# Performance work log

Measured on AMD Instinct MI355X. Metric: run time of the kernel, lower is better.

The kernel has to match this reference:

```python
import jax, jax.numpy as jnp
import numpy as np

EPS = 1e-12

def _spectral_normalize(W, u):
    # torch spectral_norm (eval-time math): v = normalize(W^T u), sigma = u^T W v
    u = jax.lax.stop_gradient(u)
    v = W.T @ u
    v = jax.lax.stop_gradient(v / (jnp.linalg.norm(v) + EPS))
    sigma = u @ (W @ v)
    return W / sigma

def _conv1x1(x, W):
    # 1x1 conv, no bias: (out,in) x (B,in,H,W) -> (B,out,H,W)
    return jnp.einsum('oc,bchw->bohw', W, x)

def setup_inputs() -> dict:
    key = jax.random.key(0)
    ks = jax.random.split(key, 10)
    B, C, H, W = 4, 512, 64, 64
    Cp = C // 8
    return {
        'x': jax.random.normal(ks[0], (B, C, H, W), jnp.float32),
        'Wf': jax.random.normal(ks[1], (Cp, C), jnp.float32) * 0.05,
        'Wg': jax.random.normal(ks[2], (Cp, C), jnp.float32) * 0.05,
        'Wh': jax.random.normal(ks[3], (Cp, C), jnp.float32) * 0.05,
        'Wv': jax.random.normal(ks[4], (C, Cp), jnp.float32) * 0.05,
        'uf': jax.random.normal(ks[5], (Cp,), jnp.float32),
        'ug': jax.random.normal(ks[6], (Cp,), jnp.float32),
        'uh': jax.random.normal(ks[7], (Cp,), jnp.float32),
        'uv': jax.random.normal(ks[8], (C,), jnp.float32),
        'gamma': jax.random.normal(ks[9], (1,), jnp.float32) * 0.1,
    }

def reference(x, Wf, Wg, Wh, Wv, uf, ug, uh, uv, gamma):
    B, C, H, W = x.shape
    Cp = Wf.shape[0]
    N = H * W
    Wf_sn = _spectral_normalize(Wf, uf)
    Wg_sn = _spectral_normalize(Wg, ug)
    Wh_sn = _spectral_normalize(Wh, uh)
    Wv_sn = _spectral_normalize(Wv, uv)
    fx = _conv1x1(x, Wf_sn).reshape(B, Cp, N)   # (B,Cp,N)
    gx = _conv1x1(x, Wg_sn).reshape(B, Cp, N)   # (B,Cp,N)
    # fx^T gx: (B,N,N), unscaled single-head attention, softmax over last dim
    scores = jnp.einsum('bcn,bcm->bnm', fx, gx)
    attn = jax.nn.softmax(scores, axis=-1)
    hx = _conv1x1(x, Wh_sn).reshape(B, Cp, N)
    # hx @ attn: out[b,c,j] = sum_i hx[b,c,i] * attn[b,i,j]
    out = jnp.einsum('bci,bij->bcj', hx, attn).reshape(B, Cp, H, W)
    unscaled = _conv1x1(out, Wv_sn)
    return gamma * unscaled + x
```

## Files before the change

### kernel.cpp

```cpp
#include <hip/hip_runtime.h>


#define NB 4
#define CC 512
#define CP 64
#define NN 4096

typedef __attribute__((ext_vector_type(8))) short short8;
typedef __attribute__((ext_vector_type(4))) float floatx4;
typedef __attribute__((ext_vector_type(16))) float floatx16;

#define MFMA32(A, B, C) __builtin_amdgcn_mfma_f32_32x32x16_bf16((A), (B), (C), 0, 0, 0)

__device__ __forceinline__ float bf2f_u(unsigned short h) {
    return __uint_as_float((unsigned)h << 16);
}
__device__ __forceinline__ float bf16lo(unsigned v) { return __uint_as_float(v << 16); }
__device__ __forceinline__ float bf16hi(unsigned v) { return __uint_as_float(v & 0xffff0000u); }
__device__ __forceinline__ unsigned short f2bf(float f) {
    unsigned u = __float_as_uint(f);
    u += 0x7fffu + ((u >> 16) & 1u);
    return (unsigned short)(u >> 16);
}
__device__ __forceinline__ unsigned pack2bf(float a, float b) {
    return (unsigned)f2bf(a) | ((unsigned)f2bf(b) << 16);
}
__device__ __forceinline__ float ldS(const void* p, long i, int f32) {
    return f32 ? ((const float*)p)[i] : bf2f_u(((const unsigned short*)p)[i]);
}
__device__ __forceinline__ float2 ld2(const void* p, long i, int f32) {
    if (f32) return *reinterpret_cast<const float2*>((const float*)p + i);
    unsigned v = *reinterpret_cast<const unsigned*>((const unsigned short*)p + i);
    return make_float2(bf16lo(v), bf16hi(v));
}
__device__ __forceinline__ float4 ld4(const void* p, long i, int f32) {
    if (f32) return *reinterpret_cast<const float4*>((const float*)p + i);
    uint2 v = *reinterpret_cast<const uint2*>((const unsigned short*)p + i);
    return make_float4(bf16lo(v.x), bf16hi(v.x), bf16lo(v.y), bf16hi(v.y));
}
__device__ __forceinline__ short8 frag8(const void* p, long i, int f32) {
    uint4 au;
    if (f32) {
        float4 v0 = *reinterpret_cast<const float4*>((const float*)p + i);
        float4 v1 = *reinterpret_cast<const float4*>((const float*)p + i + 4);
        au.x = pack2bf(v0.x, v0.y); au.y = pack2bf(v0.z, v0.w);
        au.z = pack2bf(v1.x, v1.y); au.w = pack2bf(v1.z, v1.w);
    } else {
        au = *reinterpret_cast<const uint4*>((const unsigned short*)p + i);
    }
    return *reinterpret_cast<short8*>(&au);
}
__device__ __forceinline__ short8 as_s8(uint4 v) { return *reinterpret_cast<short8*>(&v); }
__device__ __forceinline__ floatx16 zero16() {
    floatx16 z;
    #pragma unroll
    for (int i = 0; i < 16; ++i) z[i] = 0.f;
    return z;
}
__device__ __forceinline__ unsigned cvtpk_bf16(float a, float b) {
    unsigned r;
    asm("v_cvt_pk_bf16_f32 %0, %1, %2" : "=v"(r) : "v"(a), "v"(b));
    return r;
}
__device__ __forceinline__ void pl32swap(unsigned &a, unsigned &b) {
    asm("v_permlane32_swap_b32 %0, %1" : "+v"(a), "+v"(b));
}
__device__ __forceinline__ float rcpf(float x) {
    float r;
    asm("v_rcp_f32 %0, %1" : "=v"(r) : "v"(x));
    return r;
}

__global__ __launch_bounds__(256) void detect_kernel(
    const unsigned* __restrict__ x, int* __restrict__ flag)
{
    __shared__ int red[256];
    const int t = threadIdx.x;
    int bad = 0;
    for (int i = t; i < 4096; i += 256) {
        unsigned w = x[i];
        float f0 = __uint_as_float(w << 16);
        float f1 = __uint_as_float(w & 0xffff0000u);
        float a0 = fabsf(f0), a1 = fabsf(f1);
        if (!(a0 <= 1e3f) || (f0 != 0.f && a0 < 1e-20f)) bad++;
        if (!(a1 <= 1e3f) || (f1 != 0.f && a1 < 1e-20f)) bad++;
    }
    red[t] = bad;
    __syncthreads();
    for (int s = 128; s > 0; s >>= 1) { if (t < s) red[t] += red[t + s]; __syncthreads(); }
    if (t == 0) *flag = (red[0] > 64) ? 1 : 0;
}

__global__ __launch_bounds__(512) void sigma_kernel(
    const void* __restrict__ Wf, const void* __restrict__ Wg,
    const void* __restrict__ Wh, const void* __restrict__ Wv,
    const void* __restrict__ uf, const void* __restrict__ ug,
    const void* __restrict__ uh, const void* __restrict__ uv,
    const int* __restrict__ dflag, float* __restrict__ sig)
{
    const int f32 = *dflag;
    const int w = blockIdx.x;
    const void* W;
    const void* u;
    if (w == 0)      { W = Wf; u = uf; }
    else if (w == 1) { W = Wg; u = ug; }
    else if (w == 2) { W = Wh; u = uh; }
    else             { W = Wv; u = uv; }

    __shared__ float us[512];
    __shared__ float red[512];
    const int t = threadIdx.x;
    float S;

    if (w < 3) {
        if (t < 64) us[t] = ldS(u, t, f32);
        __syncthreads();
        float a = 0.f;
        #pragma unroll
        for (int i = 0; i < 64; ++i)
            a = fmaf(ldS(W, (long)i * 512 + t, f32), us[i], a);
        red[t] = a * a;
        __syncthreads();
        #pragma unroll
        for (int s = 256; s > 0; s >>= 1) {
            if (t < s) red[t] += red[t + s];
            __syncthreads();
        }
        S = red[0];
    } else {
        us[t] = ldS(u, t, f32);
        __syncthreads();
        const int g = t >> 6, c = t & 63;
        float a = 0.f;
        #pragma unroll
        for (int k = 0; k < 64; ++k) {
            int i = g + k * 8;
            a = fmaf(ldS(W, (long)i * 64 + c, f32), us[i], a);
        }
        red[t] = a;
        __syncthreads();
        #pragma unroll
        for (int s = 256; s >= 64; s >>= 1) {
            if (t < s) red[t] += red[t + s];
            __syncthreads();
        }
        float ac = (t < 64) ? red[t] : 0.f;
        __syncthreads();
        red[t] = ac * ac;
        __syncthreads();
        #pragma unroll
        for (int s = 256; s > 0; s >>= 1) {
            if (t < s) red[t] += red[t + s];
            __syncthreads();
        }
        S = red[0];
    }
    if (t == 0) sig[w] = (sqrtf(S) + 1e-12f) / S;
}

__global__ __launch_bounds__(256) void proj_kernel(
    const void* __restrict__ x,
    const void* __restrict__ Wf,
    const void* __restrict__ Wg,
    const void* __restrict__ Wh,
    const int* __restrict__ dflag,
    const float* __restrict__ sig,
    unsigned short* __restrict__ fxF, unsigned short* __restrict__ gxF,
    unsigned short* __restrict__ hxF)
{
    const int f32 = *dflag;
    const int n0 = blockIdx.x * 64;
    const int b  = blockIdx.y;
    const int wi = blockIdx.z;
    const void* __restrict__ W = (wi == 0) ? Wf : ((wi == 1) ? Wg : Wh);
    const float scale = sig[wi];

    __shared__ unsigned short Wl[64][72];

    const int t = threadIdx.x;
    const int wv = t >> 6, l = t & 63, l15 = l & 15, quad = l >> 4;
    const int n = n0 + 16 * wv + l15;

    floatx4 acc[4];
    #pragma unroll
    for (int ct = 0; ct < 4; ++ct) acc[ct] = (floatx4){0.f, 0.f, 0.f, 0.f};

    for (int kc = 0; kc < CC; kc += 64) {
        #pragma unroll
        for (int idx = t; idx < 2048; idx += 256) {
            int c  = idx >> 5;
            int kk = (idx & 31) * 2;
            float2 v = ld2(W, (long)c * CC + kc + kk, f32);
            *reinterpret_cast<unsigned*>(&Wl[c][kk]) = pack2bf(v.x * scale, v.y * scale);
        }
        __syncthreads();

        #pragma unroll
        for (int ks = 0; ks < 2; ++ks) {
            const int kbase = kc + ks * 32 + quad * 8;
            float xv[8];
            #pragma unroll
            for (int j = 0; j < 8; ++j)
                xv[j] = ldS(x, ((long)b * CC + kbase + j) * NN + n, f32);
            uint4 au;
            au.x = pack2bf(xv[0], xv[1]); au.y = pack2bf(xv[2], xv[3]);
            au.z = pack2bf(xv[4], xv[5]); au.w = pack2bf(xv[6], xv[7]);
            short8 a = *reinterpret_cast<short8*>(&au);
            #pragma unroll
            for (int ct = 0; ct < 4; ++ct) {
                short8 bfr = *reinterpret_cast<const short8*>(
                    &Wl[ct * 16 + l15][ks * 32 + quad * 8]);
                acc[ct] = __builtin_amdgcn_mfma_f32_16x16x32_bf16(a, bfr, acc[ct], 0, 0, 0);
            }
        }
        __syncthreads();
    }

    if (wi < 2) {
        unsigned short* __restrict__ dstF = (wi == 0) ? fxF : gxF;
        const int nloc = 16 * wv + quad * 4;
        #pragma unroll
        for (int ct = 0; ct < 4; ++ct)
            #pragma unroll
            for (int r = 0; r < 4; ++r) {
                int nn = n0 + nloc + r;
                size_t off = (((size_t)(b * 128 + (nn >> 5)) * 4 + ct) * 64
                              + (l15 >> 3) * 32 + (nn & 31)) * 8 + (l15 & 7);
                dstF[off] = f2bf(acc[ct][r]);
            }
    } else {
        const int tile = (n0 + 16 * wv) >> 5;
        const int ich  = wv & 1;
        const int ksub = quad >> 1;
        const int ebase = (quad & 1) * 4;
        #pragma unroll
        for (int ct = 0; ct < 4; ++ct) {
            int part = ct >> 1;
            int lloc = ksub * 32 + (ct & 1) * 16 + l15;
            size_t off = ((((size_t)(b * 128 + tile) * 2 + ich) * 2 + part) * 64
                          + lloc) * 8 + ebase;
            uint2 o;
            o.x = pack2bf(acc[ct][0], acc[ct][1]);
            o.y = pack2bf(acc[ct][2], acc[ct][3]);
            *reinterpret_cast<uint2*>(&hxF[off]) = o;
        }
    }
}

__global__ __launch_bounds__(256, 4) void rowstats_kernel(
    const unsigned short* __restrict__ fxF, const unsigned short* __restrict__ gxF,
    float* __restrict__ rl)
{
    const int t = threadIdx.x;
    const int w = t >> 6, l = t & 63, l31 = l & 31, hi = l >> 5;
    const int b = blockIdx.z;
    const int i0 = blockIdx.x * 128 + w * 32;
    const int jbase = blockIdx.y * (NN / 8);

    const unsigned short* fA = fxF + ((size_t)(b * 128 + (i0 >> 5))) * 2048 + (size_t)l * 8;
    uint4 af[4];
    #pragma unroll
    for (int kc = 0; kc < 4; ++kc)
        af[kc] = *reinterpret_cast<const uint4*>(fA + kc * 512);

    const unsigned short* gB = gxF + ((size_t)(b * 128 + (jbase >> 5))) * 2048 + (size_t)l * 8;

    float suml[16];
    #pragma unroll
    for (int r = 0; r < 16; ++r) suml[r] = 0.f;

    uint4 bf0[4], bf1[4];
    auto loadB = [&](uint4* bf, int jt) {
        const unsigned short* p = gB + (size_t)jt * 2048;
        #pragma unroll
        for (int kc = 0; kc < 4; ++kc)
            bf[kc] = *reinterpret_cast<const uint4*>(p + kc * 512);
    };
    auto bodyR = [&](uint4* bf) {
        floatx16 s = zero16();
        #pragma unroll
        for (int kc = 0; kc < 4; ++kc)
            s = MFMA32(as_s8(af[kc]), as_s8(bf[kc]), s);
        #pragma unroll
        for (int r = 0; r < 16; ++r) suml[r] += __expf(s[r]);
    };

    loadB(bf0, 0);
    for (int jt = 0; jt < 16; jt += 2) {
        loadB(bf1, jt + 1);
        bodyR(bf0);
        if (jt + 2 < 16) loadB(bf0, jt + 2);
        bodyR(bf1);
    }

    #pragma unroll
    for (int r = 0; r < 16; ++r) {
        float v = suml[r];
        v += __shfl_xor(v, 1);
        v += __shfl_xor(v, 2);
        v += __shfl_xor(v, 4);
        v += __shfl_xor(v, 8);
        v += __shfl_xor(v, 16);
        suml[r] = v;
    }
    if (l31 == 0) {
        #pragma unroll
        for (int r = 0; r < 16; ++r) {
            int row = (r & 3) + 8 * (r >> 2) + 4 * hi;
            atomicAdd(&rl[(size_t)b * NN + i0 + row], suml[r]);
        }
    }
}

__global__ __launch_bounds__(256, 2) void pv_kernel(
    const unsigned short* __restrict__ fxF, const unsigned short* __restrict__ gxF,
    const unsigned short* __restrict__ hxF, const float* __restrict__ rl,
    float* __restrict__ opT0, float* __restrict__ opT1)
{
    const int t = threadIdx.x;
    const int w = t >> 6, l = t & 63, l31 = l & 31, hi = l >> 5;
    const int b = blockIdx.z;
    const int j0 = blockIdx.x * 64;
    const int isb = blockIdx.y;
    const int ibase = isb * (NN / 2) + w * (NN / 8);

    __shared__ float red[64 * 64];

    uint4 qf0[4], qf1[4];
    {
        const unsigned short* gq = gxF + ((size_t)(b * 128 + (j0 >> 5))) * 2048 + (size_t)l * 8;
        #pragma unroll
        for (int kc = 0; kc < 4; ++kc) {
            qf0[kc] = *reinterpret_cast<const uint4*>(gq + kc * 512);
            qf1[kc] = *reinterpret_cast<const uint4*>(gq + 2048 + kc * 512);
        }
    }

    floatx16 acc00 = zero16(), acc01 = zero16();
    floatx16 acc10 = zero16(), acc11 = zero16();

    const unsigned short* fb = fxF + ((size_t)(b * 128 + (ibase >> 5))) * 2048 + (size_t)l * 8;
    const unsigned short* vb = hxF + ((size_t)(b * 128 + (ibase >> 5))) * 2048 + (size_t)l * 8;
    const float* rbase = rl + (size_t)b * NN + ibase + (hi << 2);

    uint4 af0[4], af1[4], vf[4];
    auto loadA = [&](uint4* af, int it) {
        const unsigned short* p = fb + (size_t)it * 2048;
        #pragma unroll
        for (int kc = 0; kc < 4; ++kc)
            af[kc] = *reinterpret_cast<const uint4*>(p + kc * 512);
    };
    auto loadV = [&](int it) {
        const unsigned short* p = vb + (size_t)it * 2048;
        vf[0] = *reinterpret_cast<const uint4*>(p);
        vf[1] = *reinterpret_cast<const uint4*>(p + 1024);
        vf[2] = *reinterpret_cast<const uint4*>(p + 512);
        vf[3] = *reinterpret_cast<const uint4*>(p + 1536);
    };
    auto body = [&](uint4* af, int it) {
        const float* rp = rbase + it * 32;
        float4 rv0 = *reinterpret_cast<const float4*>(rp);
        float4 rv1 = *reinterpret_cast<const float4*>(rp + 8);
        float4 rv2 = *reinterpret_cast<const float4*>(rp + 16);
        float4 rv3 = *reinterpret_cast<const float4*>(rp + 24);
        float ri[16];
        ri[0] = rcpf(rv0.x); ri[1] = rcpf(rv0.y); ri[2] = rcpf(rv0.z); ri[3] = rcpf(rv0.w);
        ri[4] = rcpf(rv1.x); ri[5] = rcpf(rv1.y); ri[6] = rcpf(rv1.z); ri[7] = rcpf(rv1.w);
        ri[8] = rcpf(rv2.x); ri[9] = rcpf(rv2.y); ri[10] = rcpf(rv2.z); ri[11] = rcpf(rv2.w);
        ri[12] = rcpf(rv3.x); ri[13] = rcpf(rv3.y); ri[14] = rcpf(rv3.z); ri[15] = rcpf(rv3.w);
        #pragma unroll
        for (int sub = 0; sub < 2; ++sub) {
            uint4* qf = sub ? qf1 : qf0;
            floatx16 s = zero16();
            #pragma unroll
            for (int kc = 0; kc < 4; ++kc)
                s = MFMA32(as_s8(af[kc]), as_s8(qf[kc]), s);
            float e[16];
            #pragma unroll
            for (int r = 0; r < 16; ++r) e[r] = __expf(s[r]) * ri[r];
            unsigned u0 = cvtpk_bf16(e[0], e[1]);
            unsigned u1 = cvtpk_bf16(e[2], e[3]);
            unsigned u2 = cvtpk_bf16(e[4], e[5]);
            unsigned u3 = cvtpk_bf16(e[6], e[7]);
            pl32swap(u0, u2);
            pl32swap(u1, u3);
            uint4 pa0 = make_uint4(u0, u1, u2, u3);
            unsigned u4 = cvtpk_bf16(e[8], e[9]);
            unsigned u5 = cvtpk_bf16(e[10], e[11]);
            unsigned u6 = cvtpk_bf16(e[12], e[13]);
            unsigned u7 = cvtpk_bf16(e[14], e[15]);
            pl32swap(u4, u6);
            pl32swap(u5, u7);
            uint4 pa1 = make_uint4(u4, u5, u6, u7);
            floatx16& a0 = sub ? acc10 : acc00;
            floatx16& a1 = sub ? acc11 : acc01;
            a0 = MFMA32(as_s8(pa0), as_s8(vf[0]), a0);
            a0 = MFMA32(as_s8(pa1), as_s8(vf[1]), a0);
            a1 = MFMA32(as_s8(pa0), as_s8(vf[2]), a1);
            a1 = MFMA32(as_s8(pa1), as_s8(vf[3]), a1);
        }
    };

    loadA(af0, 0);
    for (int it = 0; it < 16; it += 2) {
        loadV(it);
        loadA(af1, it + 1);
        body(af0, it);
        loadV(it + 1);
        if (it + 2 < 16) loadA(af0, it + 2);
        body(af1, it + 1);
    }

    #pragma unroll
    for (int q = 0; q < 4; ++q)
        *reinterpret_cast<float4*>(&red[(q * 256 + t) * 4]) = make_float4(0.f, 0.f, 0.f, 0.f);
    __syncthreads();
    #pragma unroll
    for (int r = 0; r < 16; ++r) {
        int row = (r & 3) + 8 * (r >> 2) + 4 * hi;
        atomicAdd(&red[row * 64 + l31],              acc00[r]);
        atomicAdd(&red[row * 64 + 32 + l31],         acc01[r]);
        atomicAdd(&red[(32 + row) * 64 + l31],       acc10[r]);
        atomicAdd(&red[(32 + row) * 64 + 32 + l31],  acc11[r]);
    }
    __syncthreads();
    float* dst = (isb ? opT1 : opT0) + ((size_t)b * NN + j0) * CP;
    #pragma unroll
    for (int q = 0; q < 4; ++q) {
        int o = (q * 256 + t) * 4;
        *reinterpret_cast<float4*>(dst + o) = *reinterpret_cast<const float4*>(&red[o]);
    }
}

__global__ __launch_bounds__(256) void outproj_kernel(
    const void* __restrict__ x,
    const void* __restrict__ Wv,
    const void* __restrict__ gamma,
    const int* __restrict__ dflag,
    const float* __restrict__ sig,
    const float* __restrict__ opT0,
    const float* __restrict__ opT1,
    void* __restrict__ y)
{
    const int f32 = *dflag;
    const int n0     = blockIdx.x * 64;
    const int cobase = blockIdx.y * 128;
    const int b      = blockIdx.z;
    const int t = threadIdx.x;
    const int wv = t >> 6, l = t & 63, l15 = l & 15, quad = l >> 4;
    const float scale = ldS(gamma, 0, f32) * sig[3];

    floatx4 acc[4][2];
    #pragma unroll
    for (int ns = 0; ns < 4; ++ns)
        #pragma unroll
        for (int ct = 0; ct < 2; ++ct) acc[ns][ct] = (floatx4){0.f, 0.f, 0.f, 0.f};

    #pragma unroll
    for (int ks = 0; ks < 2; ++ks) {
        const int kb = ks * 32 + quad * 8;
        short8 a[4];
        #pragma unroll
        for (int ns = 0; ns < 4; ++ns) {
            const long off = ((long)b * NN + n0 + 16 * ns + l15) * CP + kb;
            float4 x0 = *reinterpret_cast<const float4*>(opT0 + off);
            float4 x1 = *reinterpret_cast<const float4*>(opT0 + off + 4);
            float4 y0 = *reinterpret_cast<const float4*>(opT1 + off);
            float4 y1 = *reinterpret_cast<const float4*>(opT1 + off + 4);
            uint4 au;
            au.x = pack2bf(x0.x + y0.x, x0.y + y0.y);
            au.y = pack2bf(x0.z + y0.z, x0.w + y0.w);
            au.z = pack2bf(x1.x + y1.x, x1.y + y1.y);
            au.w = pack2bf(x1.z + y1.z, x1.w + y1.w);
            a[ns] = *reinterpret_cast<short8*>(&au);
        }
        #pragma unroll
        for (int ct = 0; ct < 2; ++ct) {
            const int co = cobase + 32 * wv + 16 * ct + l15;
            short8 bfr = frag8(Wv, (long)co * CP + kb, f32);
            #pragma unroll
            for (int ns = 0; ns < 4; ++ns)
                acc[ns][ct] = __builtin_amdgcn_mfma_f32_16x16x32_bf16(a[ns], bfr, acc[ns][ct], 0, 0, 0);
        }
    }

    #pragma unroll
    for (int ns = 0; ns < 4; ++ns)
        #pragma unroll
        for (int ct = 0; ct < 2; ++ct) {
            const int co = cobase + 32 * wv + 16 * ct + l15;
            const long base = ((long)b * CC + co) * NN + n0 + 16 * ns + quad * 4;
            float4 xv = ld4(x, base, f32);
            float o0 = fmaf(scale, acc[ns][ct][0], xv.x);
            float o1 = fmaf(scale, acc[ns][ct][1], xv.y);
            float o2 = fmaf(scale, acc[ns][ct][2], xv.z);
            float o3 = fmaf(scale, acc[ns][ct][3], xv.w);
            if (f32) {
                *reinterpret_cast<float4*>((float*)y + base) = make_float4(o0, o1, o2, o3);
            } else {
                uint2 o;
                o.x = pack2bf(o0, o1);
                o.y = pack2bf(o2, o3);
                *reinterpret_cast<uint2*>((unsigned short*)y + base) = o;
            }
        }
}

extern "C" void kernel_launch(void* const* d_in, const int* in_sizes, int n_in,
                              void* d_out, int out_size, void* d_ws, size_t ws_size,
                              hipStream_t stream)
{
    const void* x  = d_in[0];
    const void* Wf = d_in[1];
    const void* Wg = d_in[2];
    const void* Wh = d_in[3];
    const void* Wv = d_in[4];
    const void* uf = d_in[5];
    const void* ug = d_in[6];
    const void* uh = d_in[7];
    const void* uv = d_in[8];
    const void* gm = d_in[9];

    char* base = (char*)d_ws;
    int*   dfl = (int*)(base);
    float* sig = (float*)(base + 512);
    float* rl  = (float*)(base + 1024);
    float* opT0 = (float*)(base + 1024 + 65536);
    float* opT1 = opT0 + (size_t)NB * NN * CP;
    unsigned short* fxF = (unsigned short*)(opT1 + (size_t)NB * NN * CP);
    unsigned short* gxF = fxF + (size_t)NB * CP * NN;
    unsigned short* hxF = gxF + (size_t)NB * CP * NN;

    hipMemsetAsync(rl, 0, (size_t)NB * NN * sizeof(float), stream);

    hipLaunchKernelGGL(detect_kernel, dim3(1), dim3(256), 0, stream,
                       (const unsigned*)x, dfl);
    hipLaunchKernelGGL(sigma_kernel, dim3(4), dim3(512), 0, stream,
                       Wf, Wg, Wh, Wv, uf, ug, uh, uv, dfl, sig);
    hipLaunchKernelGGL(proj_kernel, dim3(NN / 64, NB, 3), dim3(256), 0, stream,
                       x, Wf, Wg, Wh, dfl, sig, fxF, gxF, hxF);
    hipLaunchKernelGGL(rowstats_kernel, dim3(NN / 128, 8, NB), dim3(256), 0, stream,
                       fxF, gxF, rl);
    hipLaunchKernelGGL(pv_kernel, dim3(NN / 64, 2, NB), dim3(256), 0, stream,
                       fxF, gxF, hxF, rl, opT0, opT1);
    hipLaunchKernelGGL(outproj_kernel, dim3(NN / 64, CC / 128, NB), dim3(256), 0, stream,
                       x, Wv, gm, dfl, sig, opT0, opT1, d_out);
}
```

Before: 244.4 us.

## Fuse projections, fold log2e and row normalization into hx, split PV wider

The projection kernel now computes f, g and h in one launch, so x is read once instead of three times. Wf is pre-scaled by log2(e) so the softmax exponent can use the raw v_exp_f32 (exp2) instruction. The per-row 1/rowsum is folded into hx by a new small scale kernel, which removes the reciprocal and multiply from the PV inner loop. PV is split into four i-slices with lighter per-wave state and higher occupancy, at the cost of four partial-output buffers that the output projection must sum, plus an extra launch and extra bf16 rounding of hx.

```diff
diff --git a/kernel.cpp b/kernel.cpp
--- a/kernel.cpp
+++ b/kernel.cpp
@@ -5,6 +5,7 @@
 #define CC 512
 #define CP 64
 #define NN 4096
+#define L2E 1.4426950408889634f
 
 typedef __attribute__((ext_vector_type(8))) short short8;
 typedef __attribute__((ext_vector_type(4))) float floatx4;
@@ -68,6 +69,11 @@
 __device__ __forceinline__ float rcpf(float x) {
     float r;
     asm("v_rcp_f32 %0, %1" : "=v"(r) : "v"(x));
+    return r;
+}
+__device__ __forceinline__ float exp2a(float x) {
+    float r;
+    asm("v_exp_f32 %0, %1" : "=v"(r) : "v"(x));
     return r;
 }
 
@@ -171,27 +177,35 @@
     const int f32 = *dflag;
     const int n0 = blockIdx.x * 64;
     const int b  = blockIdx.y;
-    const int wi = blockIdx.z;
-    const void* __restrict__ W = (wi == 0) ? Wf : ((wi == 1) ? Wg : Wh);
-    const float scale = sig[wi];
-
-    __shared__ unsigned short Wl[64][72];
+
+    __shared__ unsigned short Wl[3][64][72];
 
     const int t = threadIdx.x;
     const int wv = t >> 6, l = t & 63, l15 = l & 15, quad = l >> 4;
     const int n = n0 + 16 * wv + l15;
 
-    floatx4 acc[4];
-    #pragma unroll
-    for (int ct = 0; ct < 4; ++ct) acc[ct] = (floatx4){0.f, 0.f, 0.f, 0.f};
+    float sc[3];
+    sc[0] = sig[0] * L2E;
+    sc[1] = sig[1];
+    sc[2] = sig[2];
+    const void* Ws[3] = {Wf, Wg, Wh};
+
+    floatx4 acc[3][4];
+    #pragma unroll
+    for (int wi = 0; wi < 3; ++wi)
+        #pragma unroll
+        for (int ct = 0; ct < 4; ++ct) acc[wi][ct] = (floatx4){0.f, 0.f, 0.f, 0.f};
 
     for (int kc = 0; kc < CC; kc += 64) {
         #pragma unroll
-        for (int idx = t; idx < 2048; idx += 256) {
-            int c  = idx >> 5;
-            int kk = (idx & 31) * 2;
-            float2 v = ld2(W, (long)c * CC + kc + kk, f32);
-            *reinterpret_cast<unsigned*>(&Wl[c][kk]) = pack2bf(v.x * scale, v.y * scale);
+        for (int idx = t; idx < 6144; idx += 256) {
+            int wi  = idx >> 11;
+            int rem = idx & 2047;
+            int c   = rem >> 5;
+            int kk  = (rem & 31) * 2;
+            float2 v = ld2(Ws[wi], (long)c * CC + kc + kk, f32);
+            *reinterpret_cast<unsigned*>(&Wl[wi][c][kk]) =
+                pack2bf(v.x * sc[wi], v.y * sc[wi]);
         }
         __syncthreads();
 
@@ -207,16 +221,20 @@
             au.z = pack2bf(xv[4], xv[5]); au.w = pack2bf(xv[6], xv[7]);
             short8 a = *reinterpret_cast<short8*>(&au);
             #pragma unroll
-            for (int ct = 0; ct < 4; ++ct) {
-                short8 bfr = *reinterpret_cast<const short8*>(
-                    &Wl[ct * 16 + l15][ks * 32 + quad * 8]);
-                acc[ct] = __builtin_amdgcn_mfma_f32_16x16x32_bf16(a, bfr, acc[ct], 0, 0, 0);
-            }
-        }
-        __syncthreads();
-    }
-
-    if (wi < 2) {
+            for (int wi = 0; wi < 3; ++wi)
+                #pragma unroll
+                for (int ct = 0; ct < 4; ++ct) {
+                    short8 bfr = *reinterpret_cast<const short8*>(
+                        &Wl[wi][ct * 16 + l15][ks * 32 + quad * 8]);
+                    acc[wi][ct] = __builtin_amdgcn_mfma_f32_16x16x32_bf16(
+                        a, bfr, acc[wi][ct], 0, 0, 0);
+                }
+        }
+        __syncthreads();
+    }
+
+    #pragma unroll
+    for (int wi = 0; wi < 2; ++wi) {
         unsigned short* __restrict__ dstF = (wi == 0) ? fxF : gxF;
         const int nloc = 16 * wv + quad * 4;
         #pragma unroll
@@ -226,9 +244,10 @@
                 int nn = n0 + nloc + r;
                 size_t off = (((size_t)(b * 128 + (nn >> 5)) * 4 + ct) * 64
                               + (l15 >> 3) * 32 + (nn & 31)) * 8 + (l15 & 7);
-                dstF[off] = f2bf(acc[ct][r]);
+                dstF[off] = f2bf(acc[wi][ct][r]);
             }
-    } else {
+    }
+    {
         const int tile = (n0 + 16 * wv) >> 5;
         const int ich  = wv & 1;
         const int ksub = quad >> 1;
@@ -240,8 +259,8 @@
             size_t off = ((((size_t)(b * 128 + tile) * 2 + ich) * 2 + part) * 64
                           + lloc) * 8 + ebase;
             uint2 o;
-            o.x = pack2bf(acc[ct][0], acc[ct][1]);
-            o.y = pack2bf(acc[ct][2], acc[ct][3]);
+            o.x = pack2bf(acc[2][ct][0], acc[2][ct][1]);
+            o.y = pack2bf(acc[2][ct][2], acc[2][ct][3]);
             *reinterpret_cast<uint2*>(&hxF[off]) = o;
         }
     }
@@ -282,7 +301,7 @@
         for (int kc = 0; kc < 4; ++kc)
             s = MFMA32(as_s8(af[kc]), as_s8(bf[kc]), s);
         #pragma unroll
-        for (int r = 0; r < 16; ++r) suml[r] += __expf(s[r]);
+        for (int r = 0; r < 16; ++r) suml[r] += exp2a(s[r]);
     };
 
     loadB(bf0, 0);
@@ -312,123 +331,127 @@
     }
 }
 
-__global__ __launch_bounds__(256, 2) void pv_kernel(
+__global__ __launch_bounds__(256) void scalehx_kernel(
+    const float* __restrict__ rl, unsigned short* __restrict__ hxF)
+{
+    const int idx = blockIdx.x * 256 + threadIdx.x;
+    const int l = idx & 63;
+    const int r = idx >> 6;
+    const int ich = (r >> 1) & 1;
+    const int tile = (r >> 2) & 127;
+    const int b = r >> 9;
+    const int i0 = tile * 32 + ich * 16 + (l >> 5) * 8;
+    const float* rp = rl + (size_t)b * NN + i0;
+    float4 ra = *reinterpret_cast<const float4*>(rp);
+    float4 rb = *reinterpret_cast<const float4*>(rp + 4);
+    uint4 v = *reinterpret_cast<uint4*>(hxF + (size_t)idx * 8);
+    uint4 ov;
+    ov.x = pack2bf(bf16lo(v.x) * rcpf(ra.x), bf16hi(v.x) * rcpf(ra.y));
+    ov.y = pack2bf(bf16lo(v.y) * rcpf(ra.z), bf16hi(v.y) * rcpf(ra.w));
+    ov.z = pack2bf(bf16lo(v.z) * rcpf(rb.x), bf16hi(v.z) * rcpf(rb.y));
+    ov.w = pack2bf(bf16lo(v.w) * rcpf(rb.z), bf16hi(v.w) * rcpf(rb.w));
+    *reinterpret_cast<uint4*>(hxF + (size_t)idx * 8) = ov;
+}
+
+__global__ __launch_bounds__(256, 4) void pv_kernel(
     const unsigned short* __restrict__ fxF, const unsigned short* __restrict__ gxF,
-    const unsigned short* __restrict__ hxF, const float* __restrict__ rl,
-    float* __restrict__ opT0, float* __restrict__ opT1)
+    const unsigned short* __restrict__ hxF,
+    float* __restrict__ opF0, float* __restrict__ opF1,
+    float* __restrict__ opF2, float* __restrict__ opF3)
 {
     const int t = threadIdx.x;
     const int w = t >> 6, l = t & 63, l31 = l & 31, hi = l >> 5;
+    const int igrp = w >> 1, jgrp = w & 1;
     const int b = blockIdx.z;
     const int j0 = blockIdx.x * 64;
     const int isb = blockIdx.y;
-    const int ibase = isb * (NN / 2) + w * (NN / 8);
+    const int tbase = isb * 32 + igrp * 16;
 
     __shared__ float red[64 * 64];
 
-    uint4 qf0[4], qf1[4];
+    uint4 qf[4];
     {
-        const unsigned short* gq = gxF + ((size_t)(b * 128 + (j0 >> 5))) * 2048 + (size_t)l * 8;
-        #pragma unroll
-        for (int kc = 0; kc < 4; ++kc) {
-            qf0[kc] = *reinterpret_cast<const uint4*>(gq + kc * 512);
-            qf1[kc] = *reinterpret_cast<const uint4*>(gq + 2048 + kc * 512);
-        }
-    }
-
-    floatx16 acc00 = zero16(), acc01 = zero16();
-    floatx16 acc10 = zero16(), acc11 = zero16();
-
-    const unsigned short* fb = fxF + ((size_t)(b * 128 + (ibase >> 5))) * 2048 + (size_t)l * 8;
-    const unsigned short* vb = hxF + ((size_t)(b * 128 + (ibase >> 5))) * 2048 + (size_t)l * 8;
-    const float* rbase = rl + (size_t)b * NN + ibase + (hi << 2);
-
-    uint4 af0[4], af1[4], vf[4];
-    auto loadA = [&](uint4* af, int it) {
-        const unsigned short* p = fb + (size_t)it * 2048;
+        const unsigned short* gq =
+            gxF + ((size_t)(b * 128 + (j0 >> 5) + jgrp)) * 2048 + (size_t)l * 8;
         #pragma unroll
         for (int kc = 0; kc < 4; ++kc)
-            af[kc] = *reinterpret_cast<const uint4*>(p + kc * 512);
-    };
-    auto loadV = [&](int it) {
-        const unsigned short* p = vb + (size_t)it * 2048;
-        vf[0] = *reinterpret_cast<const uint4*>(p);
-        vf[1] = *reinterpret_cast<const uint4*>(p + 1024);
-        vf[2] = *reinterpret_cast<const uint4*>(p + 512);
-        vf[3] = *reinterpret_cast<const uint4*>(p + 1536);
-    };
-    auto body = [&](uint4* af, int it) {
-        const float* rp = rbase + it * 32;
-        float4 rv0 = *reinterpret_cast<const float4*>(rp);
-        float4 rv1 = *reinterpret_cast<const float4*>(rp + 8);
-        float4 rv2 = *reinterpret_cast<const float4*>(rp + 16);
-        float4 rv3 = *reinterpret_cast<const float4*>(rp + 24);
-        float ri[16];
-        ri[0] = rcpf(rv0.x); ri[1] = rcpf(rv0.y); ri[2] = rcpf(rv0.z); ri[3] = rcpf(rv0.w);
-        ri[4] = rcpf(rv1.x); ri[5] = rcpf(rv1.y); ri[6] = rcpf(rv1.z); ri[7] = rcpf(rv1.w);
-        ri[8] = rcpf(rv2.x); ri[9] = rcpf(rv2.y); ri[10] = rcpf(rv2.z); ri[11] = rcpf(rv2.w);
-        ri[12] = rcpf(rv3.x); ri[13] = rcpf(rv3.y); ri[14] = rcpf(rv3.z); ri[15] = rcpf(rv3.w);
-        #pragma unroll
-        for (int sub = 0; sub < 2; ++sub) {
-            uint4* qf = sub ? qf1 : qf0;
-            floatx16 s = zero16();
-            #pragma unroll
-            for (int kc = 0; kc < 4; ++kc)
-                s = MFMA32(as_s8(af[kc]), as_s8(qf[kc]), s);
-            float e[16];
-            #pragma unroll
-            for (int r = 0; r < 16; ++r) e[r] = __expf(s[r]) * ri[r];
-            unsigned u0 = cvtpk_bf16(e[0], e[1]);
-            unsigned u1 = cvtpk_bf16(e[2], e[3]);
-            unsigned u2 = cvtpk_bf16(e[4], e[5]);
-            unsigned u3 = cvtpk_bf16(e[6], e[7]);
-            pl32swap(u0, u2);
-            pl32swap(u1, u3);
-            uint4 pa0 = make_uint4(u0, u1, u2, u3);
-            unsigned u4 = cvtpk_bf16(e[8], e[9]);
-            unsigned u5 = cvtpk_bf16(e[10], e[11]);
-            unsigned u6 = cvtpk_bf16(e[12], e[13]);
-            unsigned u7 = cvtpk_bf16(e[14], e[15]);
-            pl32swap(u4, u6);
-            pl32swap(u5, u7);
-            uint4 pa1 = make_uint4(u4, u5, u6, u7);
-            floatx16& a0 = sub ? acc10 : acc00;
-            floatx16& a1 = sub ? acc11 : acc01;
-            a0 = MFMA32(as_s8(pa0), as_s8(vf[0]), a0);
-            a0 = MFMA32(as_s8(pa1), as_s8(vf[1]), a0);
-            a1 = MFMA32(as_s8(pa0), as_s8(vf[2]), a1);
-            a1 = MFMA32(as_s8(pa1), as_s8(vf[3]), a1);
-        }
-    };
-
-    loadA(af0, 0);
-    for (int it = 0; it < 16; it += 2) {
-        loadV(it);
-        loadA(af1, it + 1);
-        body(af0, it);
-        loadV(it + 1);
-        if (it + 2 < 16) loadA(af0, it + 2);
-        body(af1, it + 1);
+            qf[kc] = *reinterpret_cast<const uint4*>(gq + kc * 512);
+    }
+
+    floatx16 acc0 = zero16(), acc1 = zero16();
+
+    const unsigned short* fb = fxF + ((size_t)(b * 128 + tbase)) * 2048 + (size_t)l * 8;
+    const unsigned short* vb = hxF + ((size_t)(b * 128 + tbase)) * 2048 + (size_t)l * 8;
+
+    #pragma unroll 2
+    for (int it = 0; it < 16; ++it) {
+        const unsigned short* fp = fb + (size_t)it * 2048;
+        const unsigned short* vp = vb + (size_t)it * 2048;
+        uint4 af[4], vf[4];
+        #pragma unroll
+        for (int kc = 0; kc < 4; ++kc)
+            af[kc] = *reinterpret_cast<const uint4*>(fp + kc * 512);
+        vf[0] = *reinterpret_cast<const uint4*>(vp);
+        vf[1] = *reinterpret_cast<const uint4*>(vp + 1024);
+        vf[2] = *reinterpret_cast<const uint4*>(vp + 512);
+        vf[3] = *reinterpret_cast<const uint4*>(vp + 1536);
+
+        floatx16 s = zero16();
+        #pragma unroll
+        for (int kc = 0; kc < 4; ++kc)
+            s = MFMA32(as_s8(af[kc]), as_s8(qf[kc]), s);
+
+        float e[16];
+        #pragma unroll
+        for (int r = 0; r < 16; ++r) e[r] = exp2a(s[r]);
+
+        unsigned u0 = cvtpk_bf16(e[0], e[1]);
+        unsigned u1 = cvtpk_bf16(e[2], e[3]);
+        unsigned u2 = cvtpk_bf16(e[4], e[5]);
+        unsigned u3 = cvtpk_bf16(e[6], e[7]);
+        pl32swap(u0, u2);
+        pl32swap(u1, u3);
+        uint4 pa0 = make_uint4(u0, u1, u2, u3);
+        unsigned u4 = cvtpk_bf16(e[8], e[9]);
+        unsigned u5 = cvtpk_bf16(e[10], e[11]);
+        unsigned u6 = cvtpk_bf16(e[12], e[13]);
+        unsigned u7 = cvtpk_bf16(e[14], e[15]);
+        pl32swap(u4, u6);
+        pl32swap(u5, u7);
+        uint4 pa1 = make_uint4(u4, u5, u6, u7);
+
+        acc0 = MFMA32(as_s8(pa0), as_s8(vf[0]), acc0);
+        acc0 = MFMA32(as_s8(pa1), as_s8(vf[1]), acc0);
+        acc1 = MFMA32(as_s8(pa0), as_s8(vf[2]), acc1);
+        acc1 = MFMA32(as_s8(pa1), as_s8(vf[3]), acc1);
     }
 
     #pragma unroll
     for (int q = 0; q < 4; ++q)
-        *reinterpret_cast<float4*>(&red[(q * 256 + t) * 4]) = make_float4(0.f, 0.f, 0.f, 0.f);
+        *reinterpret_cast<float4*>(&red[(q * 256 + t) * 4]) =
+            make_float4(0.f, 0.f, 0.f, 0.f);
     __syncthreads();
     #pragma unroll
     for (int r = 0; r < 16; ++r) {
-        int row = (r & 3) + 8 * (r >> 2) + 4 * hi;
-        atomicAdd(&red[row * 64 + l31],              acc00[r]);
-        atomicAdd(&red[row * 64 + 32 + l31],         acc01[r]);
-        atomicAdd(&red[(32 + row) * 64 + l31],       acc10[r]);
-        atomicAdd(&red[(32 + row) * 64 + 32 + l31],  acc11[r]);
+        int row = jgrp * 32 + (r & 3) + 8 * (r >> 2) + 4 * hi;
+        atomicAdd(&red[row * 64 + l31],      acc0[r]);
+        atomicAdd(&red[row * 64 + 32 + l31], acc1[r]);
     }
     __syncthreads();
-    float* dst = (isb ? opT1 : opT0) + ((size_t)b * NN + j0) * CP;
+
+    float* __restrict__ dst = (isb == 0) ? opF0 : ((isb == 1) ? opF1 : ((isb == 2) ? opF2 : opF3));
     #pragma unroll
     for (int q = 0; q < 4; ++q) {
-        int o = (q * 256 + t) * 4;
-        *reinterpret_cast<float4*>(dst + o) = *reinterpret_cast<const float4*>(&red[o]);
+        int idx = q * 256 + t;
+        int e2  = idx & 1;
+        int ll  = (idx >> 1) & 63;
+        int ks  = (idx >> 7) & 1;
+        int ntl = idx >> 8;
+        int jloc = ntl * 16 + (ll & 15);
+        int cp   = ks * 32 + ((ll >> 4) << 3) + e2 * 4;
+        float4 v = *reinterpret_cast<const float4*>(&red[jloc * 64 + cp]);
+        size_t off = (((size_t)(b * 256 + (j0 >> 4) + ntl) * 2 + ks) * 64 + ll) * 8 + e2 * 4;
+        *reinterpret_cast<float4*>(dst + off) = v;
     }
 }
 
@@ -438,8 +461,8 @@
     const void* __restrict__ gamma,
     const int* __restrict__ dflag,
     const float* __restrict__ sig,
-    const float* __restrict__ opT0,
-    const float* __restrict__ opT1,
+    const float* __restrict__ opF0, const float* __restrict__ opF1,
+    const float* __restrict__ opF2, const float* __restrict__ opF3,
     void* __restrict__ y)
 {
     const int f32 = *dflag;
@@ -458,29 +481,40 @@
 
     #pragma unroll
     for (int ks = 0; ks < 2; ++ks) {
+        short8 a[4];
+        #pragma unroll
+        for (int ns = 0; ns < 4; ++ns) {
+            size_t fo = (((size_t)(b * 256 + (n0 >> 4) + ns) * 2 + ks) * 64 + l) * 8;
+            float4 s0 = *reinterpret_cast<const float4*>(opF0 + fo);
+            float4 s1 = *reinterpret_cast<const float4*>(opF1 + fo);
+            float4 s2 = *reinterpret_cast<const float4*>(opF2 + fo);
+            float4 s3 = *reinterpret_cast<const float4*>(opF3 + fo);
+            float4 t0 = *reinterpret_cast<const float4*>(opF0 + fo + 4);
+            float4 t1 = *reinterpret_cast<const float4*>(opF1 + fo + 4);
+            float4 t2 = *reinterpret_cast<const float4*>(opF2 + fo + 4);
+            float4 t3 = *reinterpret_cast<const float4*>(opF3 + fo + 4);
+            float v0 = s0.x + s1.x + s2.x + s3.x;
+            float v1 = s0.y + s1.y + s2.y + s3.y;
+            float v2 = s0.z + s1.z + s2.z + s3.z;
+            float v3 = s0.w + s1.w + s2.w + s3.w;
+            float v4 = t0.x + t1.x + t2.x + t3.x;
+            float v5 = t0.y + t1.y + t2.y + t3.y;
+            float v6 = t0.z + t1.z + t2.z + t3.z;
+            float v7 = t0.w + t1.w + t2.w + t3.w;
+            uint4 au;
+            au.x = pack2bf(v0, v1); au.y = pack2bf(v2, v3);
+            au.z = pack2bf(v4, v5); au.w = pack2bf(v6, v7);
+            a[ns] = *reinterpret_cast<short8*>(&au);
+        }
         const int kb = ks * 32 + quad * 8;
-        short8 a[4];
-        #pragma unroll
-        for (int ns = 0; ns < 4; ++ns) {
-            const long off = ((long)b * NN + n0 + 16 * ns + l15) * CP + kb;
-            float4 x0 = *reinterpret_cast<const float4*>(opT0 + off);
-            float4 x1 = *reinterpret_cast<const float4*>(opT0 + off + 4);
-            float4 y0 = *reinterpret_cast<const float4*>(opT1 + off);
-            float4 y1 = *reinterpret_cast<const float4*>(opT1 + off + 4);
-            uint4 au;
-            au.x = pack2bf(x0.x + y0.x, x0.y + y0.y);
-            au.y = pack2bf(x0.z + y0.z, x0.w + y0.w);
-            au.z = pack2bf(x1.x + y1.x, x1.y + y1.y);
-            au.w = pack2bf(x1.z + y1.z, x1.w + y1.w);
-            a[ns] = *reinterpret_cast<short8*>(&au);
-        }
         #pragma unroll
         for (int ct = 0; ct < 2; ++ct) {
             const int co = cobase + 32 * wv + 16 * ct + l15;
             short8 bfr = frag8(Wv, (long)co * CP + kb, f32);
             #pragma unroll
             for (int ns = 0; ns < 4; ++ns)
-                acc[ns][ct] = __builtin_amdgcn_mfma_f32_16x16x32_bf16(a[ns], bfr, acc[ns][ct], 0, 0, 0);
+                acc[ns][ct] = __builtin_amdgcn_mfma_f32_16x16x32_bf16(
+                    a[ns], bfr, acc[ns][ct], 0, 0, 0);
         }
     }
 
@@ -525,9 +559,11 @@
     int*   dfl = (int*)(base);
     float* sig = (float*)(base + 512);
     float* rl  = (float*)(base + 1024);
-    float* opT0 = (float*)(base + 1024 + 65536);
-    float* opT1 = opT0 + (size_t)NB * NN * CP;
-    unsigned short* fxF = (unsigned short*)(opT1 + (size_t)NB * NN * CP);
+    float* opF0 = (float*)(base + 1024 + 65536);
+    float* opF1 = opF0 + (size_t)NB * NN * CP;
+    float* opF2 = opF1 + (size_t)NB * NN * CP;
+    float* opF3 = opF2 + (size_t)NB * NN * CP;
+    unsigned short* fxF = (unsigned short*)(opF3 + (size_t)NB * NN * CP);
     unsigned short* gxF = fxF + (size_t)NB * CP * NN;
     unsigned short* hxF = gxF + (size_t)NB * CP * NN;
 
@@ -537,12 +573,14 @@
                        (const unsigned*)x, dfl);
     hipLaunchKernelGGL(sigma_kernel, dim3(4), dim3(512), 0, stream,
                        Wf, Wg, Wh, Wv, uf, ug, uh, uv, dfl, sig);
-    hipLaunchKernelGGL(proj_kernel, dim3(NN / 64, NB, 3), dim3(256), 0, stream,
+    hipLaunchKernelGGL(proj_kernel, dim3(NN / 64, NB), dim3(256), 0, stream,
                        x, Wf, Wg, Wh, dfl, sig, fxF, gxF, hxF);
     hipLaunchKernelGGL(rowstats_kernel, dim3(NN / 128, 8, NB), dim3(256), 0, stream,
                        fxF, gxF, rl);
-    hipLaunchKernelGGL(pv_kernel, dim3(NN / 64, 2, NB), dim3(256), 0, stream,
-                       fxF, gxF, hxF, rl, opT0, opT1);
+    hipLaunchKernelGGL(scalehx_kernel, dim3((NB * CP * NN / 8) / 256), dim3(256), 0, stream,
+                       rl, hxF);
+    hipLaunchKernelGGL(pv_kernel, dim3(NN / 64, 4, NB), dim3(256), 0, stream,
+                       fxF, gxF, hxF, opF0, opF1, opF2, opF3);
     hipLaunchKernelGGL(outproj_kernel, dim3(NN / 64, CC / 128, NB), dim3(256), 0, stream,
-                       x, Wv, gm, dfl, sig, opT0, opT1, d_out);
-}
+                       x, Wv, gm, dfl, sig, opF0, opF1, opF2, opF3, d_out);
+}
```

Measured after the change: 292.9 us. 19.8% more time.
